# Performance work log

Hardware: AMD Instinct MI355X
Metric: run time of the kernel (lower is better)

The kernel has to match this reference:

```python
import jax, jax.numpy as jnp
import numpy as np

H, P, G, N, K, CS = 64, 64, 8, 128, 4, 256
HID = 2048
INTER = H * P                      # 4096
CONV_D = INTER + 2 * G * N         # 6144
PROJ = INTER + CONV_D + H          # 10304
EPS = 1e-5


def setup_inputs() -> dict:
    key = jax.random.key(0)
    ks = jax.random.split(key, 4)
    B_, L_ = 2, 2048
    return {
        "hidden_states": jax.random.normal(ks[0], (B_, L_, HID), jnp.float32),
        "in_proj_w": jax.random.normal(ks[1], (PROJ, HID), jnp.float32) * 0.02,
        "conv_w": jax.random.normal(ks[2], (CONV_D, K), jnp.float32) * 0.2,
        "conv_b": jnp.zeros((CONV_D,), jnp.float32),
        "dt_bias": jnp.ones((H,), jnp.float32),
        "A_log": jnp.log(jnp.arange(1, H + 1, dtype=jnp.float32)),
        "D": jnp.ones((H,), jnp.float32),
        "norm_w": jnp.ones((INTER,), jnp.float32),
        "out_proj_w": jax.random.normal(ks[3], (HID, INTER), jnp.float32) * 0.02,
    }


def reference(hidden_states, in_proj_w, conv_w, conv_b, dt_bias, A_log, D, norm_w, out_proj_w):
    b, l, _ = hidden_states.shape
    r = H // G  # heads per group

    zxbcdt = hidden_states @ in_proj_w.T                      # [b,l,PROJ]
    z = zxbcdt[..., :INTER]
    xBC = zxbcdt[..., INTER:INTER + CONV_D]
    dt = zxbcdt[..., INTER + CONV_D:]                          # [b,l,H]

    # causal depthwise conv1d (kernel K, left pad K-1) + SiLU
    xp = jnp.pad(xBC, ((0, 0), (K - 1, 0), (0, 0)))
    conv = conv_b
    for i in range(K):
        conv = conv + conv_w[:, i] * xp[:, i:i + l, :]
    xBC = jax.nn.silu(conv)

    x = xBC[..., :INTER]
    Bm = xBC[..., INTER:INTER + G * N]
    Cm = xBC[..., INTER + G * N:]

    dt = jax.nn.softplus(dt + dt_bias)                         # [b,l,H]
    A = -jnp.exp(A_log)                                        # [H]

    nc = l // CS
    x_c = x.reshape(b, nc, CS, G, r, P)
    dt_c = dt.reshape(b, nc, CS, G, r)
    B_c = Bm.reshape(b, nc, CS, G, N)
    C_c = Cm.reshape(b, nc, CS, G, N)

    dA = dt_c * A.reshape(G, r)                                # [b,nc,c,g,r]
    dA_cs = jnp.cumsum(dA, axis=2)                             # inclusive cumsum over chunk

    # intra-chunk: L[i,j] = exp(dA_cs[i]-dA_cs[j]) for i>=j
    diff = dA_cs[:, :, :, None] - dA_cs[:, :, None]            # [b,nc,i,j,g,r]
    mask = jnp.tril(jnp.ones((CS, CS), bool))[None, None, :, :, None, None]
    Lmat = jnp.exp(jnp.where(mask, diff, -jnp.inf))
    CB = jnp.einsum('bzign,bzjgn->bzijg', C_c, B_c)            # per-group C·B
    M = CB[..., None] * Lmat * dt_c[:, :, None]                # [b,nc,i,j,g,r]
    Y_diag = jnp.einsum('bzijgr,bzjgrp->bzigrp', M, x_c)

    # per-chunk end states
    w = jnp.exp(dA_cs[:, :, -1:] - dA_cs) * dt_c               # decay to chunk end * dt
    states = jnp.einsum('bzjgn,bzjgr,bzjgrp->bzgrpn', B_c, w, x_c)  # [b,nc,g,r,p,n]
    chunk_decay = jnp.exp(dA_cs[:, :, -1])                     # [b,nc,g,r]

    def step(S, inp):
        d, s = inp
        return d[..., None, None] * S + s, S                   # emit state BEFORE chunk

    init = jnp.zeros((b, G, r, P, N), x.dtype)
    _, prev = jax.lax.scan(step, init, (jnp.moveaxis(chunk_decay, 1, 0), jnp.moveaxis(states, 1, 0)))
    prev = jnp.moveaxis(prev, 0, 1)                            # [b,nc,g,r,p,n]

    Y_off = jnp.einsum('bzign,bzgrpn->bzigrp', C_c, prev) * jnp.exp(dA_cs)[..., None]

    Y = (Y_diag + Y_off).reshape(b, l, H, P) + D[:, None] * x.reshape(b, l, H, P)
    y = Y.reshape(b, l, INTER)

    # gated RMSNorm, norm_before_gate=True: out = rmsnorm(y) * silu(z)
    var = jnp.mean(y * y, axis=-1, keepdims=True)
    y = norm_w * (y * jax.lax.rsqrt(var + EPS)) * jax.nn.silu(z)

    return y @ out_proj_w.T
```

## Files before the change

kernel.cpp:

```cpp
#include <hip/hip_runtime.h>
#include <hip/hip_bf16.h>
#include <cstdint>
#include <cstddef>

#define H_     64
#define P_     64
#define G_     8
#define N_     128
#define K_     4
#define CS_    256
#define HID_   2048
#define INTER_ 4096
#define CONVD_ 6144
#define PROJ_  10304
#define ZSTR_  10240
#define B_     2
#define L_     2048
#define NC_    8
#define ML_    4096
#define EPS_   1e-5f

typedef unsigned short ushort_t;
typedef __attribute__((ext_vector_type(8))) short short8;
typedef __attribute__((ext_vector_type(4))) float f32x4;

__device__ inline float b2f(ushort_t v) {
  unsigned u = ((unsigned)v) << 16;
  float f;
  __builtin_memcpy(&f, &u, 4);
  return f;
}
__device__ inline ushort_t f2b(float f) {
  unsigned u;
  __builtin_memcpy(&u, &f, 4);
  u = u + 0x7FFFu + ((u >> 16) & 1u);
  return (ushort_t)(u >> 16);
}
__device__ inline void ld_bf8(const ushort_t* p, float* f) {
  uint4 u = *(const uint4*)p;
  const ushort_t* s = (const ushort_t*)&u;
#pragma unroll
  for (int c = 0; c < 8; ++c) f[c] = b2f(s[c]);
}
__device__ inline void st_bf8(ushort_t* p, const float* f) {
  uint4 u;
  ushort_t* s = (ushort_t*)&u;
#pragma unroll
  for (int c = 0; c < 8; ++c) s[c] = f2b(f[c]);
  *(uint4*)p = u;
}

__global__ __launch_bounds__(256) void cast1_k(const float* __restrict__ hs,
                                               const float* __restrict__ w_in,
                                               ushort_t* __restrict__ hsb,
                                               ushort_t* __restrict__ w_inb) {
  size_t e8 = ((size_t)blockIdx.x * 256 + threadIdx.x) * 8;
  const float* src;
  ushort_t* dst;
  const size_t HSN = (size_t)ML_ * HID_;
  if (e8 < HSN) { src = hs + e8; dst = hsb + e8; }
  else          { src = w_in + (e8 - HSN); dst = w_inb + (e8 - HSN); }
  float4 a = *(const float4*)src;
  float4 b = *(const float4*)(src + 4);
  float v[8] = {a.x, a.y, a.z, a.w, b.x, b.y, b.z, b.w};
  st_bf8(dst, v);
}

typedef const __attribute__((address_space(1))) unsigned int gu32;
typedef __attribute__((address_space(3))) unsigned int lu32;
__device__ __forceinline__ void gl_lds16(const ushort_t* g, ushort_t* l) {
  __builtin_amdgcn_global_load_lds((gu32*)g, (lu32*)l, 16, 0, 0);
}

template<int N> __device__ __forceinline__ void wait_vmcnt() {
  if constexpr (N == 8)      asm volatile("s_waitcnt vmcnt(8)" ::: "memory");
  else if constexpr (N == 6) asm volatile("s_waitcnt vmcnt(6)" ::: "memory");
  else if constexpr (N == 4) asm volatile("s_waitcnt vmcnt(4)" ::: "memory");
  else if constexpr (N == 3) asm volatile("s_waitcnt vmcnt(3)" ::: "memory");
  else                       asm volatile("s_waitcnt vmcnt(0)" ::: "memory");
}

template<int MR>
__device__ __forceinline__ void gemm_core(const ushort_t* __restrict__ Ag,
                                          const ushort_t* __restrict__ Bg,
                                          int lda, int ldb, int nkt,
                                          int bm, int bn, int brmax,
                                          ushort_t* __restrict__ As,
                                          ushort_t* __restrict__ Bs,
                                          f32x4 (&acc)[MR / 32][4]) {
  constexpr int MF = MR / 32;
  constexpr int ASLOT = MR * 32;
  constexpr int BSLOT = 256 * 32;
  constexpr int LPT = (MR == 256) ? 4 : 3;
  const int t = threadIdx.x;
  const int w = t >> 6, l = t & 63;
  const int wm = w >> 2, wn = w & 3;
  const int ml = l & 15, q = l >> 4;
  const int swz = (ml >> 1) & 3;
  const int aoff = (wm * (MR / 2) + ml) * 32 + ((q ^ swz) << 3);
  const int boff = (wn * 64 + ml) * 32 + ((q ^ swz) << 3);
  const int permc = (((l & 3) ^ ((l >> 3) & 3)) << 3);
  const ushort_t* ag0 = Ag + (size_t)(bm + (MR / 8) * w + (l >> 2)) * lda + permc;
  const ushort_t* ag1 = ag0 + (size_t)16 * lda;
  int br0 = bn + 32 * w + (l >> 2);      if (br0 > brmax) br0 = brmax;
  int br1 = bn + 32 * w + 16 + (l >> 2); if (br1 > brmax) br1 = brmax;
  const ushort_t* bg0 = Bg + (size_t)br0 * ldb + permc;
  const ushort_t* bg1 = Bg + (size_t)br1 * ldb + permc;
  ushort_t* alw = As + ((MR == 256) ? (2 * w * 512) : (w * 512));
  ushort_t* blw = Bs + 2 * w * 512;

#define STAGE_A_(kt_)                                                        \
  { const int k_ = (kt_) << 5;                                               \
    ushort_t* sa_ = alw + ((kt_) & 3) * ASLOT;                               \
    gl_lds16(ag0 + k_, sa_);                                                 \
    if (MR == 256) gl_lds16(ag1 + k_, sa_ + 512); }
#define STAGE_B_(kt_)                                                        \
  { const int k_ = (kt_) << 5;                                               \
    ushort_t* sb_ = blw + ((kt_) & 3) * BSLOT;                               \
    gl_lds16(bg0 + k_, sb_);                                                 \
    gl_lds16(bg1 + k_, sb_ + 512); }

  STAGE_A_(0); STAGE_B_(0);
  STAGE_A_(1); STAGE_B_(1);
  STAGE_A_(2); STAGE_B_(2);

#pragma unroll
  for (int i = 0; i < MF; ++i)
#pragma unroll
    for (int j = 0; j < 4; ++j) acc[i][j] = (f32x4){0.f, 0.f, 0.f, 0.f};

#pragma unroll 1
  for (int kt = 0; kt < nkt; ++kt) {
    const ushort_t* Asl = As + (kt & 3) * ASLOT;
    const ushort_t* Bsl = Bs + (kt & 3) * BSLOT;
    if (kt + 2 < nkt)      wait_vmcnt<2 * LPT>();
    else if (kt + 1 < nkt) wait_vmcnt<LPT>();
    else                   wait_vmcnt<0>();
    __builtin_amdgcn_s_barrier();
    asm volatile("" ::: "memory");
    const bool st = (kt + 3) < nkt;
    short8 bfr[4], af[MF / 2];
#pragma unroll
    for (int nf = 0; nf < 4; ++nf)
      bfr[nf] = *(const short8*)(Bsl + boff + nf * 512);
#pragma unroll
    for (int mf = 0; mf < MF / 2; ++mf)
      af[mf] = *(const short8*)(Asl + aoff + mf * 512);
    if (st) STAGE_A_(kt + 3);
    __builtin_amdgcn_s_setprio(1);
#pragma unroll
    for (int mf = 0; mf < MF / 2; ++mf)
#pragma unroll
      for (int nf = 0; nf < 4; ++nf)
        acc[mf][nf] = __builtin_amdgcn_mfma_f32_16x16x32_bf16(af[mf], bfr[nf], acc[mf][nf], 0, 0, 0);
    __builtin_amdgcn_s_setprio(0);
#pragma unroll
    for (int mf = 0; mf < MF / 2; ++mf)
      af[mf] = *(const short8*)(Asl + aoff + (mf + MF / 2) * 512);
    if (st) STAGE_B_(kt + 3);
    __builtin_amdgcn_s_setprio(1);
#pragma unroll
    for (int mf = 0; mf < MF / 2; ++mf)
#pragma unroll
      for (int nf = 0; nf < 4; ++nf)
        acc[mf + MF / 2][nf] = __builtin_amdgcn_mfma_f32_16x16x32_bf16(af[mf], bfr[nf], acc[mf + MF / 2][nf], 0, 0, 0);
    __builtin_amdgcn_s_setprio(0);
  }
#undef STAGE_A_
#undef STAGE_B_
}

__global__ __launch_bounds__(512, 2) void gemm1_256(const ushort_t* __restrict__ hsb,
                                                    const ushort_t* __restrict__ w_inb,
                                                    ushort_t* __restrict__ zb,
                                                    float* __restrict__ dtraw) {
  __shared__ __align__(16) ushort_t As[4 * 8192];
  __shared__ __align__(16) ushort_t Bs[4 * 8192];
  int bid = blockIdx.x;
  int wg = (bid & 7) * 82 + (bid >> 3);
  int tm = wg & 15, tn = wg >> 4;
  int bm = tm * 256, bn = tn * 256;
  f32x4 acc[8][4];
  gemm_core<256>(hsb, w_inb, HID_, HID_, HID_ / 32, bm, bn, PROJ_ - 1, As, Bs, acc);
  int t = threadIdx.x, w = t >> 6, l = t & 63;
  int wm = w >> 2, wn = w & 3, ml = l & 15, quad = l >> 4;
  int rb = bm + wm * 128 + quad * 4;
  int cb = bn + wn * 64 + ml;
  if (tn < 40) {
#pragma unroll
    for (int mf = 0; mf < 8; ++mf)
#pragma unroll
      for (int r = 0; r < 4; ++r) {
        size_t row = (size_t)(rb + mf * 16 + r) * ZSTR_;
#pragma unroll
        for (int nf = 0; nf < 4; ++nf)
          zb[row + cb + nf * 16] = f2b(acc[mf][nf][r]);
      }
  } else if (wn == 0) {
#pragma unroll
    for (int mf = 0; mf < 8; ++mf)
#pragma unroll
      for (int r = 0; r < 4; ++r) {
        int tok = rb + mf * 16 + r;
#pragma unroll
        for (int nf = 0; nf < 4; ++nf)
          dtraw[(size_t)(ml + nf * 16) * ML_ + tok] = acc[mf][nf][r];
      }
  }
}

__global__ __launch_bounds__(512, 2) void gemm2_128(const ushort_t* __restrict__ Ab,
                                                    const ushort_t* __restrict__ Bb,
                                                    float* __restrict__ C) {
  __shared__ __align__(16) ushort_t As[4 * 4096];
  __shared__ __align__(16) ushort_t Bs[4 * 8192];
  int bid = blockIdx.x;
  int wg = (bid & 7) * 32 + (bid >> 3);
  int tm = wg & 31, tn = wg >> 5;
  int bm = tm * 128, bn = tn * 256;
  f32x4 acc[4][4];
  gemm_core<128>(Ab, Bb, CONVD_, INTER_, INTER_ / 32, bm, bn, HID_ - 1, As, Bs, acc);
  int t = threadIdx.x, w = t >> 6, l = t & 63;
  int wm = w >> 2, wn = w & 3, ml = l & 15, quad = l >> 4;
  int rb = bm + wm * 64 + quad * 4;
  int cb = bn + wn * 64 + ml;
#pragma unroll
  for (int mf = 0; mf < 4; ++mf)
#pragma unroll
    for (int r = 0; r < 4; ++r) {
      size_t row = (size_t)(rb + mf * 16 + r) * HID_;
#pragma unroll
      for (int nf = 0; nf < 4; ++nf)
        C[row + cb + nf * 16] = acc[mf][nf][r];
    }
}

#define CROWS_ 8
__global__ __launch_bounds__(256) void conv_dt_k(const ushort_t* __restrict__ zb,
                                                 const float* __restrict__ cw,
                                                 const float* __restrict__ cb,
                                                 ushort_t* __restrict__ xcb,
                                                 const float* __restrict__ dtraw,
                                                 const float* __restrict__ dt_bias,
                                                 const float* __restrict__ A_log,
                                                 float* __restrict__ dtp,
                                                 float* __restrict__ dacs,
                                                 float* __restrict__ cdec) {
  __shared__ float sm[256];
  int bid = blockIdx.x;
  if (bid < 1536) {
    int grp = bid & 511;
    int seg = bid >> 9;
    int u = threadIdx.x;
    int c8 = seg * 2048 + u * 8;
    int row0 = grp * CROWS_;
    int l0 = row0 & (L_ - 1);

    float wv[K_][8], bias[8];
    {
      const float4* wp = (const float4*)(cw + (size_t)c8 * K_);
#pragma unroll
      for (int c = 0; c < 8; ++c) {
        float4 w4 = wp[c];
        wv[0][c] = w4.x; wv[1][c] = w4.y; wv[2][c] = w4.z; wv[3][c] = w4.w;
      }
      float4 b0 = *(const float4*)(cb + c8);
      float4 b1 = *(const float4*)(cb + c8 + 4);
      bias[0] = b0.x; bias[1] = b0.y; bias[2] = b0.z; bias[3] = b0.w;
      bias[4] = b1.x; bias[5] = b1.y; bias[6] = b1.z; bias[7] = b1.w;
    }
    const ushort_t* xin = zb + (size_t)row0 * ZSTR_ + INTER_ + c8;
    ushort_t* xout = xcb + (size_t)row0 * CONVD_ + c8;

    float win[4][8];
#pragma unroll
    for (int i = 0; i < 3; ++i) {
      if (l0 > 0) {
        ld_bf8(xin + (ptrdiff_t)(i - 3) * ZSTR_, win[i]);
      } else {
#pragma unroll
        for (int c = 0; c < 8; ++c) win[i][c] = 0.f;
      }
    }
#pragma unroll
    for (int r = 0; r < CROWS_; ++r) {
      ld_bf8(xin + (size_t)r * ZSTR_, win[(r + 3) & 3]);
      float a[8];
#pragma unroll
      for (int c = 0; c < 8; ++c) {
        float v = bias[c];
        v = fmaf(wv[0][c], win[(r + 0) & 3][c], v);
        v = fmaf(wv[1][c], win[(r + 1) & 3][c], v);
        v = fmaf(wv[2][c], win[(r + 2) & 3][c], v);
        v = fmaf(wv[3][c], win[(r + 3) & 3][c], v);
        a[c] = v / (1.f + __expf(-v));
      }
      st_bf8(xout + (size_t)r * CONVD_, a);
    }
  } else {
    int bzh = bid - 1536;
    int h = bzh & 63, z = (bzh >> 6) & 7, b = bzh >> 9;
    int i = threadIdx.x;
    size_t row = (size_t)b * L_ + z * CS_ + i;
    float dv = dtraw[(size_t)h * ML_ + row] + dt_bias[h];
    float sp = (dv > 20.f) ? dv : log1pf(expf(dv));
    float v = sp * (-expf(A_log[h]));
    sm[i] = v;
    __syncthreads();
    for (int off = 1; off < 256; off <<= 1) {
      float add = (i >= off) ? sm[i - off] : 0.f;
      __syncthreads();
      sm[i] += add;
      __syncthreads();
    }
    float cs = sm[i];
    size_t ob = ((size_t)b * H_ + h) * L_ + z * CS_ + i;
    dtp[ob] = sp;
    dacs[ob] = cs;
    if (i == CS_ - 1) cdec[bzh] = expf(cs);
  }
}

__global__ __launch_bounds__(256) void cb_k(const ushort_t* __restrict__ xcb,
                                            ushort_t* __restrict__ CBo) {
  static const unsigned char itab[10] = {0, 1, 1, 2, 2, 2, 3, 3, 3, 3};
  static const unsigned char jtab[10] = {0, 0, 1, 0, 1, 2, 0, 1, 2, 3};
  int tp = blockIdx.x;
  int it = itab[tp], jt = jtab[tp];
  int bzg = blockIdx.y;
  int g = bzg & 7, z = (bzg >> 3) & 7, b = bzg >> 6;
  int t = threadIdx.x;
  int w = t >> 6, l = t & 63;
  __shared__ __align__(16) ushort_t Cs[64 * 128];
  __shared__ __align__(16) ushort_t Bs[64 * 128];
  size_t rowbase = (size_t)b * L_ + (size_t)z * CS_;
  {
    int s = l & 15;
    int cO = INTER_ + G_ * N_ + g * N_;
    int bO = INTER_ + g * N_;
#pragma unroll
    for (int i = 0; i < 4; ++i) {
      int row = 16 * w + 4 * i + (l >> 4);
      int src = ((s ^ (row & 15)) << 3);
      gl_lds16(xcb + (rowbase + it * 64 + row) * CONVD_ + cO + src,
               Cs + (16 * w + 4 * i) * 128);
      gl_lds16(xcb + (rowbase + jt * 64 + row) * CONVD_ + bO + src,
               Bs + (16 * w + 4 * i) * 128);
    }
  }
  asm volatile("s_waitcnt vmcnt(0)" ::: "memory");
  __builtin_amdgcn_s_barrier();
  int wm = w >> 1, wn = w & 1;
  int ml = l & 15, q = l >> 4;
  f32x4 acc[2][2];
#pragma unroll
  for (int i = 0; i < 2; ++i)
#pragma unroll
    for (int j = 0; j < 2; ++j) acc[i][j] = (f32x4){0.f, 0.f, 0.f, 0.f};
#pragma unroll
  for (int kk = 0; kk < 4; ++kk) {
    short8 af[2], bf[2];
#pragma unroll
    for (int mf = 0; mf < 2; ++mf) {
      int row = wm * 32 + mf * 16 + ml;
      af[mf] = *(const short8*)(Cs + row * 128 + (((kk * 4 + q) ^ (row & 15)) << 3));
    }
#pragma unroll
    for (int nf = 0; nf < 2; ++nf) {
      int row = wn * 32 + nf * 16 + ml;
      bf[nf] = *(const short8*)(Bs + row * 128 + (((kk * 4 + q) ^ (row & 15)) << 3));
    }
#pragma unroll
    for (int mf = 0; mf < 2; ++mf)
#pragma unroll
      for (int nf = 0; nf < 2; ++nf)
        acc[mf][nf] = __builtin_amdgcn_mfma_f32_16x16x32_bf16(af[mf], bf[nf], acc[mf][nf], 0, 0, 0);
  }
  size_t cbase = ((size_t)((b * 8 + z) * 8 + g)) * (CS_ * CS_);
#pragma unroll
  for (int mf = 0; mf < 2; ++mf)
#pragma unroll
    for (int nf = 0; nf < 2; ++nf)
#pragma unroll
      for (int r = 0; r < 4; ++r) {
        int i = wm * 32 + mf * 16 + q * 4 + r;
        int j = wn * 32 + nf * 16 + ml;
        CBo[cbase + (size_t)(it * 64 + i) * CS_ + jt * 64 + j] = f2b(acc[mf][nf][r]);
      }
}

__global__ __launch_bounds__(256) void states_mfma(const ushort_t* __restrict__ xcb,
                                                   const float* __restrict__ dacs,
                                                   const float* __restrict__ dtp,
                                                   float* __restrict__ st) {
  int bzh = blockIdx.x;
  int h = bzh & 63, z = (bzh >> 6) & 7, b = bzh >> 9;
  int g = h >> 3;
  int t = threadIdx.x;
  int wv = t >> 6, lane = t & 63;
  int ml = lane & 15, ko = (lane >> 4) * 8;
  __shared__ float ws[256];
  __shared__ __align__(16) ushort_t Xw[64 * 136];
  __shared__ __align__(16) ushort_t Bt[128 * 136];
  size_t base = ((size_t)b * H_ + h) * L_ + z * CS_;
  float dlast = dacs[base + CS_ - 1];
  ws[t] = __expf(dlast - dacs[base + t]) * dtp[base + t];
  size_t rowbase = (size_t)b * L_ + z * CS_;
  f32x4 acc[4][2];
#pragma unroll
  for (int i = 0; i < 4; ++i) {
    acc[i][0] = (f32x4){0.f, 0.f, 0.f, 0.f};
    acc[i][1] = (f32x4){0.f, 0.f, 0.f, 0.f};
  }
  for (int half = 0; half < 2; ++half) {
    int j0 = half * 128;
    __syncthreads();
    {
      int j2 = (t & 63) * 2, pseg = (t >> 6) * 16;
      const ushort_t* xr0 = xcb + (rowbase + j0 + j2) * CONVD_ + h * P_ + pseg;
      const ushort_t* xr1 = xr0 + CONVD_;
      float w0 = ws[j0 + j2], w1 = ws[j0 + j2 + 1];
      float v0[8], v0b[8], v1[8], v1b[8];
      ld_bf8(xr0, v0); ld_bf8(xr0 + 8, v0b);
      ld_bf8(xr1, v1); ld_bf8(xr1 + 8, v1b);
      unsigned* xw32 = (unsigned*)Xw;
      int col = t & 63;
#pragma unroll
      for (int pp = 0; pp < 8; ++pp) {
        unsigned lo = f2b(v0[pp] * w0), hi = f2b(v1[pp] * w1);
        xw32[(pseg + pp) * 68 + col] = lo | (hi << 16);
      }
#pragma unroll
      for (int pp = 0; pp < 8; ++pp) {
        unsigned lo = f2b(v0b[pp] * w0), hi = f2b(v1b[pp] * w1);
        xw32[(pseg + 8 + pp) * 68 + col] = lo | (hi << 16);
      }
    }
    {
      int j2 = (t & 63) * 2, nseg = (t >> 6) * 32;
      const ushort_t* br0 = xcb + (rowbase + j0 + j2) * CONVD_ + INTER_ + g * N_ + nseg;
      const ushort_t* br1 = br0 + CONVD_;
      unsigned* bt32 = (unsigned*)Bt;
      int col = t & 63;
#pragma unroll
      for (int qq = 0; qq < 4; ++qq) {
        uint4 r0 = *(const uint4*)(br0 + qq * 8);
        uint4 r1 = *(const uint4*)(br1 + qq * 8);
        const ushort_t* s0 = (const ushort_t*)&r0;
        const ushort_t* s1 = (const ushort_t*)&r1;
#pragma unroll
        for (int c = 0; c < 8; ++c)
          bt32[(nseg + qq * 8 + c) * 68 + col] = (unsigned)s0[c] | ((unsigned)s1[c] << 16);
      }
    }
    __syncthreads();
#pragma unroll
    for (int k0 = 0; k0 < 128; k0 += 32) {
      short8 af[4], bf2[2];
#pragma unroll
      for (int mf = 0; mf < 4; ++mf)
        af[mf] = *(const short8*)(Xw + (mf * 16 + ml) * 136 + k0 + ko);
#pragma unroll
      for (int nf = 0; nf < 2; ++nf)
        bf2[nf] = *(const short8*)(Bt + (wv * 32 + nf * 16 + ml) * 136 + k0 + ko);
#pragma unroll
      for (int mf = 0; mf < 4; ++mf)
#pragma unroll
        for (int nf = 0; nf < 2; ++nf)
          acc[mf][nf] = __builtin_amdgcn_mfma_f32_16x16x32_bf16(af[mf], bf2[nf], acc[mf][nf], 0, 0, 0);
    }
  }
  float* outp = st + ((size_t)((b * 8 + z) * H_ + h)) * (P_ * N_);
  int quad = lane >> 4;
#pragma unroll
  for (int mf = 0; mf < 4; ++mf)
#pragma unroll
    for (int nf = 0; nf < 2; ++nf) {
      int n = wv * 32 + nf * 16 + ml;
#pragma unroll
      for (int r = 0; r < 4; ++r) {
        int p = mf * 16 + quad * 4 + r;
        outp[(size_t)p * N_ + n] = acc[mf][nf][r];
      }
    }
}

__global__ __launch_bounds__(256) void scan_k(float* __restrict__ st,
                                              const float* __restrict__ cdec) {
  size_t idx = (size_t)blockIdx.x * 256 + threadIdx.x;
  int b = (int)(idx >> 19);
  size_t rem = idx & 524287;
  int h = (int)(rem >> 13);
  float S = 0.f;
#pragma unroll
  for (int z = 0; z < NC_; ++z) {
    size_t off = (size_t)(b * 8 + z) * 524288 + rem;
    float old = st[off];
    st[off] = S;
    S = cdec[(b * 8 + z) * H_ + h] * S + old;
  }
}

__global__ __launch_bounds__(256) void y_mfma(const ushort_t* xcb,
                                              const ushort_t* __restrict__ CB,
                                              const float* __restrict__ pv,
                                              const float* __restrict__ dacs,
                                              const float* __restrict__ dtp,
                                              const float* __restrict__ Dw,
                                              ushort_t* Yx) {
  int bzh = blockIdx.x;
  int h = bzh & 63, z = (bzh >> 6) & 7, b = bzh >> 9;
  int g = h >> 3;
  int t = threadIdx.x;
  int wv = t >> 6, lane = t & 63;
  int ml = lane & 15, quad = lane >> 4, ko = quad * 8;
  __shared__ __align__(16) ushort_t Ms[256 * 40];
  __shared__ __align__(16) ushort_t XsYs[18432];
  __shared__ __align__(16) ushort_t Ps[64 * 136];
  __shared__ float dAs[256], dts[256];

  size_t rowbase = (size_t)b * L_ + z * CS_;
  {
    size_t base = ((size_t)b * H_ + h) * L_ + z * CS_;
    dAs[t] = dacs[base + t];
    dts[t] = dtp[base + t];
  }
  {
    int p = t >> 2, c0 = (t & 3) * 32;
    const float* pr = pv + ((size_t)((b * 8 + z) * H_ + h)) * (P_ * N_) + (size_t)p * N_ + c0;
    ushort_t* dst = Ps + p * 136 + c0;
#pragma unroll
    for (int u = 0; u < 4; ++u) {
      float4 a = *(const float4*)(pr + u * 8);
      float4 bq = *(const float4*)(pr + u * 8 + 4);
      float v[8] = {a.x, a.y, a.z, a.w, bq.x, bq.y, bq.z, bq.w};
      st_bf8(dst + u * 8, v);
    }
  }
  {
    const ushort_t* xr = xcb + (rowbase + t) * CONVD_ + h * P_;
    ushort_t* Xs = XsYs;
#pragma unroll
    for (int q = 0; q < 8; ++q) {
      uint4 raw = *(const uint4*)(xr + q * 8);
      const ushort_t* s = (const ushort_t*)&raw;
#pragma unroll
      for (int c = 0; c < 8; ++c) Xs[(q * 8 + c) * 264 + t] = s[c];
    }
  }

  f32x4 acc[4][4];
#pragma unroll
  for (int i = 0; i < 4; ++i)
#pragma unroll
    for (int j = 0; j < 4; ++j) acc[i][j] = (f32x4){0.f, 0.f, 0.f, 0.f};

  int cOff = INTER_ + G_ * N_ + g * N_;
#pragma unroll
  for (int k0 = 0; k0 < 128; k0 += 32) {
    __syncthreads();
#pragma unroll
    for (int u = 0; u < 4; ++u) {
      int sid = u * 256 + t;
      int row = sid >> 2, kc = (sid & 3) * 8;
      gl_lds16(xcb + (rowbase + row) * CONVD_ + cOff + k0 + kc,
               Ms + (size_t)(u * 256 + wv * 64) * 8);
    }
    __syncthreads();
    short8 af[4], bf[4];
#pragma unroll
    for (int mf = 0; mf < 4; ++mf)
      af[mf] = *(const short8*)(Ps + (mf * 16 + ml) * 136 + k0 + ko);
#pragma unroll
    for (int nf = 0; nf < 4; ++nf)
      bf[nf] = *(const short8*)(Ms + (wv * 64 + nf * 16 + ml) * 32 + ko);
#pragma unroll
    for (int mf = 0; mf < 4; ++mf)
#pragma unroll
      for (int nf = 0; nf < 4; ++nf)
        acc[mf][nf] = __builtin_amdgcn_mfma_f32_16x16x32_bf16(af[mf], bf[nf], acc[mf][nf], 0, 0, 0);
  }
#pragma unroll
  for (int nf = 0; nf < 4; ++nf) {
    float e = __expf(dAs[wv * 64 + nf * 16 + ml]);
#pragma unroll
    for (int mf = 0; mf < 4; ++mf) {
      acc[mf][nf][0] *= e; acc[mf][nf][1] *= e;
      acc[mf][nf][2] *= e; acc[mf][nf][3] *= e;
    }
  }

  float dAi_t = dAs[t];
  size_t cbase = ((size_t)((b * 8 + z) * 8 + g)) * (CS_ * CS_) + (size_t)t * CS_;
  const ushort_t* Xs = XsYs;
  uint4 pre[4];
  {
    const ushort_t* cbr = CB + cbase;
#pragma unroll
    for (int qq = 0; qq < 4; ++qq) pre[qq] = *(const uint4*)(cbr + qq * 8);
  }
  for (int j0 = 0; j0 < 256; j0 += 32) {
    __syncthreads();
    {
      ushort_t* mrow = Ms + t * 40;
#pragma unroll
      for (int qq = 0; qq < 4; ++qq) {
        const ushort_t* s = (const ushort_t*)&pre[qq];
        float o[8];
#pragma unroll
        for (int c = 0; c < 8; ++c) {
          int j = j0 + qq * 8 + c;
          float m = b2f(s[c]) * __expf(dAi_t - dAs[j]) * dts[j];
          o[c] = (j <= t) ? m : 0.f;
        }
        st_bf8(mrow + qq * 8, o);
      }
    }
    uint4 nxt[4];
    if (j0 + 32 < 256) {
      const ushort_t* cbr = CB + cbase + j0 + 32;
#pragma unroll
      for (int qq = 0; qq < 4; ++qq) nxt[qq] = *(const uint4*)(cbr + qq * 8);
    }
    __syncthreads();
    short8 af[4], bf[4];
#pragma unroll
    for (int mf = 0; mf < 4; ++mf)
      af[mf] = *(const short8*)(Xs + (mf * 16 + ml) * 264 + j0 + ko);
#pragma unroll
    for (int nf = 0; nf < 4; ++nf)
      bf[nf] = *(const short8*)(Ms + (wv * 64 + nf * 16 + ml) * 40 + ko);
#pragma unroll
    for (int mf = 0; mf < 4; ++mf)
#pragma unroll
      for (int nf = 0; nf < 4; ++nf)
        acc[mf][nf] = __builtin_amdgcn_mfma_f32_16x16x32_bf16(af[mf], bf[nf], acc[mf][nf], 0, 0, 0);
#pragma unroll
    for (int qq = 0; qq < 4; ++qq) pre[qq] = nxt[qq];
  }

  __syncthreads();
  ushort_t* Ys = XsYs;
#pragma unroll
  for (int mf = 0; mf < 4; ++mf)
#pragma unroll
    for (int nf = 0; nf < 4; ++nf) {
      int iw = wv * 64 + nf * 16 + ml;
      int pb = mf * 16 + quad * 4;
      uint2 pk;
      ushort_t* s = (ushort_t*)&pk;
      s[0] = f2b(acc[mf][nf][0]); s[1] = f2b(acc[mf][nf][1]);
      s[2] = f2b(acc[mf][nf][2]); s[3] = f2b(acc[mf][nf][3]);
      *(uint2*)(Ys + iw * 72 + pb) = pk;
    }
  __syncthreads();
  {
    float Dh = Dw[h];
    const ushort_t* xr = xcb + (rowbase + t) * CONVD_ + h * P_;
    ushort_t* yr = Yx + (rowbase + t) * CONVD_ + h * P_;
#pragma unroll
    for (int q = 0; q < 8; ++q) {
      float xv[8], yv[8], o[8];
      ld_bf8(xr + q * 8, xv);
      ld_bf8(Ys + t * 72 + q * 8, yv);
#pragma unroll
      for (int c = 0; c < 8; ++c) o[c] = yv[c] + Dh * xv[c];
      st_bf8(yr + q * 8, o);
    }
  }
}

__global__ __launch_bounds__(256) void rms_cast2_k(ushort_t* __restrict__ Y,
                                                   const ushort_t* __restrict__ zb,
                                                   const float* __restrict__ nw,
                                                   const float* __restrict__ w_out,
                                                   ushort_t* __restrict__ w_outb) {
  __shared__ float red[4];
  int bid = blockIdx.x;
  int t = threadIdx.x;
  if (bid >= ML_) {
    size_t e8 = ((size_t)(bid - ML_) * 256 + t) * 8;
    float4 a = *(const float4*)(w_out + e8);
    float4 b = *(const float4*)(w_out + e8 + 4);
    float v[8] = {a.x, a.y, a.z, a.w, b.x, b.y, b.z, b.w};
    st_bf8(w_outb + e8, v);
    return;
  }
  int row = bid;
  ushort_t* y = Y + (size_t)row * CONVD_;
  const ushort_t* zp = zb + (size_t)row * ZSTR_;
  float v[2][8];
  float s = 0.f;
#pragma unroll
  for (int u = 0; u < 2; ++u) {
    ld_bf8(y + u * 2048 + t * 8, v[u]);
#pragma unroll
    for (int c = 0; c < 8; ++c) s += v[u][c] * v[u][c];
  }
#pragma unroll
  for (int off = 32; off > 0; off >>= 1) s += __shfl_down(s, off);
  if ((t & 63) == 0) red[t >> 6] = s;
  __syncthreads();
  float tot = red[0] + red[1] + red[2] + red[3];
  float rstd = rsqrtf(tot * (1.f / INTER_) + EPS_);
#pragma unroll
  for (int u = 0; u < 2; ++u) {
    int c0 = u * 2048 + t * 8;
    float zv[8], o[8];
    ld_bf8(zp + c0, zv);
    float4 w0 = *(const float4*)(nw + c0);
    float4 w1 = *(const float4*)(nw + c0 + 4);
    float wv[8] = {w0.x, w0.y, w0.z, w0.w, w1.x, w1.y, w1.z, w1.w};
#pragma unroll
    for (int c = 0; c < 8; ++c)
      o[c] = wv[c] * v[u][c] * rstd * (zv[c] / (1.f + __expf(-zv[c])));
    st_bf8(y + c0, o);
  }
}

extern "C" void kernel_launch(void* const* d_in, const int* in_sizes, int n_in,
                              void* d_out, int out_size, void* d_ws, size_t ws_size,
                              hipStream_t stream) {
  const float* hs    = (const float*)d_in[0];
  const float* w_in  = (const float*)d_in[1];
  const float* cw    = (const float*)d_in[2];
  const float* cb    = (const float*)d_in[3];
  const float* dtb   = (const float*)d_in[4];
  const float* alog  = (const float*)d_in[5];
  const float* Dw    = (const float*)d_in[6];
  const float* nw    = (const float*)d_in[7];
  const float* w_out = (const float*)d_in[8];
  float* out = (float*)d_out;

  char* base = (char*)d_ws;
  ushort_t* zb    = (ushort_t*)(base);
  ushort_t* xcb   = (ushort_t*)(base + 83886080);
  float*    dtraw = (float*)(base + 134217728);
  float*    dtp   = (float*)(base + 135266304);
  float*    dacs  = (float*)(base + 136314880);
  float*    cdec  = (float*)(base + 137363456);
  char*     R1    = base + 137367552;
  char*     R2    = base + 154144768;
  ushort_t* hsb    = (ushort_t*)R1;
  ushort_t* cbuf   = (ushort_t*)R1;
  ushort_t* w_outb = (ushort_t*)R1;
  ushort_t* w_inb  = (ushort_t*)R2;
  float*    st     = (float*)R2;

  cast1_k<<<14400, 256, 0, stream>>>(hs, w_in, hsb, w_inb);
  gemm1_256<<<656, 512, 0, stream>>>(hsb, w_inb, zb, dtraw);
  conv_dt_k<<<2560, 256, 0, stream>>>(zb, cw, cb, xcb, dtraw, dtb, alog, dtp, dacs, cdec);
  cb_k<<<dim3(10, B_ * NC_ * G_), 256, 0, stream>>>(xcb, cbuf);
  states_mfma<<<B_ * NC_ * H_, 256, 0, stream>>>(xcb, dacs, dtp, st);
  scan_k<<<(B_ * H_ * P_ * N_) / 256, 256, 0, stream>>>(st, cdec);
  y_mfma<<<B_ * NC_ * H_, 256, 0, stream>>>(xcb, cbuf, st, dacs, dtp, Dw, xcb);
  rms_cast2_k<<<8192, 256, 0, stream>>>(xcb, zb, nw, w_out, w_outb);
  gemm2_128<<<256, 512, 0, stream>>>(xcb, w_outb, out);
}
```

Baseline: 627.3 us.

## Retile out-projection GEMM to 128x128 with triple-buffered LDS; use wave-shuffle cumsum

The output-projection GEMM moves from 128x256 tiles with 512 threads to 128x128 tiles with 256 threads. It gets its own triple-buffered LDS pipeline (global-to-LDS loads issued two k-steps ahead, swizzled fragment reads) and doubles the grid to 512 blocks, aiming for better CU occupancy and load balance. Separately, the dt chunk cumsum replaces a barrier-heavy Hillis-Steele scan in LDS with a wave-level shuffle scan plus a small cross-wave prefix. Smaller tiles give less reuse per block, and the custom pipeline depends on the vmcnt wait counts being correct.

```diff
diff --git a/kernel.cpp b/kernel.cpp
--- a/kernel.cpp
+++ b/kernel.cpp
@@ -209,21 +209,70 @@
   }
 }
 
-__global__ __launch_bounds__(512, 2) void gemm2_128(const ushort_t* __restrict__ Ab,
-                                                    const ushort_t* __restrict__ Bb,
-                                                    float* __restrict__ C) {
-  __shared__ __align__(16) ushort_t As[4 * 4096];
-  __shared__ __align__(16) ushort_t Bs[4 * 8192];
+__global__ __launch_bounds__(256, 2) void gemm2_sq(const ushort_t* __restrict__ Ab,
+                                                   const ushort_t* __restrict__ Bb,
+                                                   float* __restrict__ C) {
+  __shared__ __align__(16) ushort_t As[3 * 4096];
+  __shared__ __align__(16) ushort_t Bs[3 * 4096];
   int bid = blockIdx.x;
-  int wg = (bid & 7) * 32 + (bid >> 3);
+  int wg = (bid & 7) * 64 + (bid >> 3);
   int tm = wg & 31, tn = wg >> 5;
-  int bm = tm * 128, bn = tn * 256;
+  int bm = tm * 128, bn = tn * 128;
+  const int t = threadIdx.x;
+  const int w = t >> 6, l = t & 63;
+  const int wm = w >> 1, wn = w & 1;
+  const int ml = l & 15, q = l >> 4;
+  const int swz = (ml >> 1) & 3;
+  const int aoff = (wm * 64 + ml) * 32 + ((q ^ swz) << 3);
+  const int boff = (wn * 64 + ml) * 32 + ((q ^ swz) << 3);
+  const int permc = (((t & 3) ^ ((t >> 3) & 3)) << 3);
+  const ushort_t* ag0 = Ab + (size_t)(bm + (t >> 2)) * CONVD_ + permc;
+  const ushort_t* ag1 = Ab + (size_t)(bm + 64 + (t >> 2)) * CONVD_ + permc;
+  const ushort_t* bg0 = Bb + (size_t)(bn + (t >> 2)) * INTER_ + permc;
+  const ushort_t* bg1 = Bb + (size_t)(bn + 64 + (t >> 2)) * INTER_ + permc;
+#define STG2_(kt_)                                                           \
+  { const int sl_ = (kt_) % 3; const int k_ = (kt_) << 5;                    \
+    gl_lds16(ag0 + k_, As + sl_ * 4096 + (16 * w) * 32);                     \
+    gl_lds16(ag1 + k_, As + sl_ * 4096 + (64 + 16 * w) * 32);                \
+    gl_lds16(bg0 + k_, Bs + sl_ * 4096 + (16 * w) * 32);                     \
+    gl_lds16(bg1 + k_, Bs + sl_ * 4096 + (64 + 16 * w) * 32); }
+
   f32x4 acc[4][4];
-  gemm_core<128>(Ab, Bb, CONVD_, INTER_, INTER_ / 32, bm, bn, HID_ - 1, As, Bs, acc);
-  int t = threadIdx.x, w = t >> 6, l = t & 63;
-  int wm = w >> 2, wn = w & 3, ml = l & 15, quad = l >> 4;
-  int rb = bm + wm * 64 + quad * 4;
-  int cb = bn + wn * 64 + ml;
+#pragma unroll
+  for (int i = 0; i < 4; ++i)
+#pragma unroll
+    for (int j = 0; j < 4; ++j) acc[i][j] = (f32x4){0.f, 0.f, 0.f, 0.f};
+
+  STG2_(0);
+  STG2_(1);
+  constexpr int NKT = INTER_ / 32;
+#pragma unroll 1
+  for (int kt = 0; kt < NKT; ++kt) {
+    const ushort_t* Asl = As + (kt % 3) * 4096;
+    const ushort_t* Bsl = Bs + (kt % 3) * 4096;
+    if (kt + 1 < NKT) wait_vmcnt<4>();
+    else              wait_vmcnt<0>();
+    __builtin_amdgcn_s_barrier();
+    asm volatile("" ::: "memory");
+    short8 af[4], bf[4];
+#pragma unroll
+    for (int mf = 0; mf < 4; ++mf)
+      af[mf] = *(const short8*)(Asl + aoff + mf * 512);
+#pragma unroll
+    for (int nf = 0; nf < 4; ++nf)
+      bf[nf] = *(const short8*)(Bsl + boff + nf * 512);
+    if (kt + 2 < NKT) STG2_(kt + 2);
+    __builtin_amdgcn_s_setprio(1);
+#pragma unroll
+    for (int mf = 0; mf < 4; ++mf)
+#pragma unroll
+      for (int nf = 0; nf < 4; ++nf)
+        acc[mf][nf] = __builtin_amdgcn_mfma_f32_16x16x32_bf16(af[mf], bf[nf], acc[mf][nf], 0, 0, 0);
+    __builtin_amdgcn_s_setprio(0);
+  }
+#undef STG2_
+  int rb = bm + wm * 64 + q * 4;
+  int cbc = bn + wn * 64 + ml;
 #pragma unroll
   for (int mf = 0; mf < 4; ++mf)
 #pragma unroll
@@ -231,7 +280,7 @@
       size_t row = (size_t)(rb + mf * 16 + r) * HID_;
 #pragma unroll
       for (int nf = 0; nf < 4; ++nf)
-        C[row + cb + nf * 16] = acc[mf][nf][r];
+        C[row + cbc + nf * 16] = acc[mf][nf][r];
     }
 }
 
@@ -246,7 +295,7 @@
                                                  float* __restrict__ dtp,
                                                  float* __restrict__ dacs,
                                                  float* __restrict__ cdec) {
-  __shared__ float sm[256];
+  __shared__ float sm[4];
   int bid = blockIdx.x;
   if (bid < 1536) {
     int grp = bid & 511;
@@ -304,16 +353,20 @@
     size_t row = (size_t)b * L_ + z * CS_ + i;
     float dv = dtraw[(size_t)h * ML_ + row] + dt_bias[h];
     float sp = (dv > 20.f) ? dv : log1pf(expf(dv));
-    float v = sp * (-expf(A_log[h]));
-    sm[i] = v;
+    float s = sp * (-expf(A_log[h]));
+    int lane = i & 63;
+#pragma unroll
+    for (int off = 1; off < 64; off <<= 1) {
+      float uo = __shfl_up(s, off);
+      if (lane >= off) s += uo;
+    }
+    if (lane == 63) sm[i >> 6] = s;
     __syncthreads();
-    for (int off = 1; off < 256; off <<= 1) {
-      float add = (i >= off) ? sm[i - off] : 0.f;
-      __syncthreads();
-      sm[i] += add;
-      __syncthreads();
-    }
-    float cs = sm[i];
+    float pre = 0.f;
+#pragma unroll
+    for (int w2 = 0; w2 < 3; ++w2)
+      if (w2 < (i >> 6)) pre += sm[w2];
+    float cs = s + pre;
     size_t ob = ((size_t)b * H_ + h) * L_ + z * CS_ + i;
     dtp[ob] = sp;
     dacs[ob] = cs;
@@ -755,5 +808,5 @@
   scan_k<<<(B_ * H_ * P_ * N_) / 256, 256, 0, stream>>>(st, cdec);
   y_mfma<<<B_ * NC_ * H_, 256, 0, stream>>>(xcb, cbuf, st, dacs, dtp, Dw, xcb);
   rms_cast2_k<<<8192, 256, 0, stream>>>(xcb, zb, nw, w_out, w_outb);
-  gemm2_128<<<256, 512, 0, stream>>>(xcb, w_outb, out);
-}
+  gemm2_sq<<<512, 256, 0, stream>>>(xcb, w_outb, out);
+}
```

After: 608.2 us. 1.03x faster.
